# Performance work log

Hardware: AMD Instinct MI355X
Metric: run time of the kernel (lower is better)

Reference implementation:

```python
import jax, jax.numpy as jnp
import numpy as np

EPS = 1e-7
B, N, DIM, NH, HD, WIN, HASH_WIN = 2, 1024, 512, 8, 64, 64, 8


def expmap0(v, c):
    sqrt_c = jnp.clip(jnp.sqrt(c), EPS)
    v_norm = jnp.linalg.norm(v, axis=-1, keepdims=True)
    is_zero = v_norm < EPS
    safe = jnp.clip(v_norm, EPS)
    mag = jnp.tanh(sqrt_c * safe) / sqrt_c
    return jnp.where(is_zero, jnp.zeros_like(v), mag * (v / safe))


def poincare_dist(x, y, c):
    # x: (B,H,N,1,D), y: (B,H,N,W,D), c: (B,1,1,1,1) -> (B,H,N,W)
    sqrt_c = jnp.clip(jnp.sqrt(c), EPS)
    x2 = jnp.sum(x * x, -1, keepdims=True)
    y2 = jnp.sum(y * y, -1, keepdims=True)
    xy = jnp.sum(x * y, -1, keepdims=True)
    num = (1 - 2 * c * xy + c * y2) * x + (1 - c * x2) * (-y)
    den = 1 - 2 * c * xy + c * c * x2 * y2
    diff = num / jnp.clip(den, EPS)
    dn = jnp.linalg.norm(diff, axis=-1)
    arg = jnp.minimum(jnp.squeeze(sqrt_c, -1) * jnp.clip(dn, EPS), 1.0 - EPS)
    return 2.0 * jnp.arctanh(arg) / jnp.squeeze(sqrt_c, -1)


def sliding_windows(t, w):
    # t: (B,H,N,D) -> (B,H,N,w,D), left-padded causal window
    Bb, H, Nn, D = t.shape
    pad = jnp.zeros((Bb, H, w - 1, D), t.dtype)
    tp = jnp.concatenate([pad, t], axis=2)
    idx = jnp.arange(w)[None, :] + jnp.arange(Nn)[:, None]  # (N,w)
    return tp[:, :, idx, :]


def layernorm(x, s, b):
    m = jnp.mean(x, -1, keepdims=True)
    v = jnp.var(x, -1, keepdims=True)
    return (x - m) / jnp.sqrt(v + 1e-6) * s + b


def rope(x, cos, sin):
    # x: (B,N,H,hd), cos/sin: (N, hd//2) -- complex rotation in real arithmetic
    xr, xi = jnp.split(x, 2, axis=-1)
    cos = cos[None, :, None, :]
    sin = sin[None, :, None, :]
    return jnp.concatenate([xr * cos - xi * sin, xr * sin + xi * cos], axis=-1)


def setup_inputs() -> dict:
    key = jax.random.key(0)
    ks = jax.random.split(key, 10)
    x = jax.random.normal(ks[0], (B, N, DIM), jnp.float32)
    pos = jnp.arange(N, dtype=jnp.float32)
    inv = 1.0 / (10000.0 ** (jnp.arange(0, HD, 2, dtype=jnp.float32) / HD))
    ang = pos[:, None] * inv[None, :]  # (N, HD//2)
    freqs_cos, freqs_sin = jnp.cos(ang), jnp.sin(ang)
    c = jax.random.uniform(ks[1], (B,), jnp.float32) * 0.9 + 0.1
    s = 0.02
    Wq = jax.random.normal(ks[2], (DIM, DIM), jnp.float32) * s
    Wk = jax.random.normal(ks[3], (DIM, DIM), jnp.float32) * s
    Wv = jax.random.normal(ks[4], (DIM, DIM), jnp.float32) * s
    Wo = jax.random.normal(ks[5], (DIM, DIM), jnp.float32) * s
    W1 = jax.random.normal(ks[6], (DIM, 4 * DIM), jnp.float32) * s
    W2 = jax.random.normal(ks[7], (4 * DIM, DIM), jnp.float32) * s
    bq = jnp.zeros((DIM,)); bk = jnp.zeros((DIM,)); bv = jnp.zeros((DIM,))
    bo = jnp.zeros((DIM,)); b1 = jnp.zeros((4 * DIM,)); b2 = jnp.zeros((DIM,))
    ln1_s = jnp.ones((DIM,)); ln1_b = jnp.zeros((DIM,))
    ln2_s = jnp.ones((DIM,)); ln2_b = jnp.zeros((DIM,))
    geo_scale = jnp.ones((NH, 1, 1), jnp.float32)
    hash_offset = jax.random.normal(ks[8], (1, 1, NH, HD), jnp.float32) * 0.01
    return dict(x=x, freqs_cos=freqs_cos, freqs_sin=freqs_sin, c=c,
                Wq=Wq, bq=bq, Wk=Wk, bk=bk, Wv=Wv, bv=bv, Wo=Wo, bo=bo,
                W1=W1, b1=b1, W2=W2, b2=b2,
                ln1_s=ln1_s, ln1_b=ln1_b, ln2_s=ln2_s, ln2_b=ln2_b,
                geo_scale=geo_scale, hash_offset=hash_offset)


def reference(x, freqs_cos, freqs_sin, c, Wq, bq, Wk, bk, Wv, bv, Wo, bo,
              W1, b1, W2, b2, ln1_s, ln1_b, ln2_s, ln2_b, geo_scale, hash_offset):
    x_res = x
    xn = layernorm(x, ln1_s, ln1_b)
    q = (xn @ Wq + bq).reshape(B, N, NH, HD)
    k = (xn @ Wk + bk).reshape(B, N, NH, HD)
    v = (xn @ Wv + bv).reshape(B, N, NH, HD)
    q = q + hash_offset * jnp.log(1.0 + HASH_WIN)
    q_rot = rope(q, freqs_cos, freqs_sin)
    k_rot = rope(k, freqs_cos, freqs_sin)
    c_b = c.reshape(B, 1, 1, 1)
    q_h = expmap0(q_rot, c_b)
    k_h = expmap0(k_rot, c_b)
    q_h, k_h, v = (t.transpose(0, 2, 1, 3) for t in (q_h, k_h, v))  # (B,H,N,D)
    k_win = sliding_windows(k_h, WIN)  # (B,H,N,W,D)
    v_win = sliding_windows(v, WIN)
    dist = poincare_dist(q_h[:, :, :, None, :], k_win, c.reshape(B, 1, 1, 1, 1))  # (B,H,N,W)
    scores = -geo_scale * dist
    w = jax.nn.softmax(scores, axis=-1)
    attn = jnp.einsum('bhnw,bhnwd->bhnd', w, v_win)
    attn = attn.transpose(0, 2, 1, 3).reshape(B, N, DIM)
    x_out = x_res + (attn @ Wo + bo)
    h = layernorm(x_out, ln2_s, ln2_b)
    ffn = jax.nn.gelu(h @ W1 + b1) @ W2 + b2
    return x_out + ffn
```

## Files before the change

### kernel.cpp

```cpp
#include <hip/hip_runtime.h>
#include <math.h>
#include <stdint.h>

#define Bn   2
#define Nn   1024
#define DIMn 512
#define NHn  8
#define HDn  64
#define QKVS 1536
#define EPSF 1e-7f

typedef __attribute__((ext_vector_type(8))) short short8;
typedef __attribute__((ext_vector_type(4))) float floatx4;
typedef __attribute__((ext_vector_type(4))) float fx4;
typedef __attribute__((ext_vector_type(4))) unsigned short usx4;

__device__ __forceinline__ unsigned short f2bf(float f) {
  union { float f; uint32_t u; } v; v.f = f;
  uint32_t u = v.u;
  return (unsigned short)((u + 0x7FFFu + ((u >> 16) & 1u)) >> 16);
}
__device__ __forceinline__ float bf2f(unsigned short h) {
  union { uint32_t u; float f; } v; v.u = ((uint32_t)h) << 16;
  return v.f;
}

__device__ __forceinline__ float wsum(float v) {
#pragma unroll
  for (int m = 32; m >= 1; m >>= 1) v += __shfl_xor(v, m, 64);
  return v;
}

__device__ __forceinline__ float gelu_tanh(float x) {
  const float k0 = 0.7978845608028654f;
  float x3 = x * x * x;
  return 0.5f * x * (1.f + tanhf(k0 * (x + 0.044715f * x3)));
}

__device__ __forceinline__ void glds16(const unsigned short* g, unsigned short* l) {
  __builtin_amdgcn_global_load_lds((const __attribute__((address_space(1))) void*)g,
                                   (__attribute__((address_space(3))) void*)l, 16, 0, 0);
}

__global__ __launch_bounds__(256) void prep_kernel(
    const float* __restrict__ Wq, const float* __restrict__ Wk,
    const float* __restrict__ Wv, const float* __restrict__ Wo,
    const float* __restrict__ W1, const float* __restrict__ W2,
    unsigned short* __restrict__ Wcat_hi, unsigned short* __restrict__ Wcat_lo,
    unsigned short* __restrict__ Wo_t, unsigned short* __restrict__ W1_t,
    unsigned short* __restrict__ W2_t,
    const float* __restrict__ bq, const float* __restrict__ bk,
    const float* __restrict__ bv, float* __restrict__ bias_cat,
    const float* __restrict__ x, const float* __restrict__ ln1s,
    const float* __restrict__ ln1b,
    unsigned short* __restrict__ xn_hi, unsigned short* __restrict__ xn_lo) {
  __shared__ float t[32][33];
  __shared__ float red[2][4];
  int bid = blockIdx.x;
  int tid = threadIdx.x;
  if (bid == 3072) {
    for (int i = tid; i < 512; i += 256) {
      bias_cat[i] = bq[i];
      bias_cat[512 + i] = bk[i];
      bias_cat[1024 + i] = bv[i];
    }
    return;
  }
  if (bid > 3072) {
    int row = bid - 3073;
    const float* xr = x + (size_t)row * DIMn;
    float2 xv = *(const float2*)(xr + tid * 2);
    float s  = xv.x + xv.y;
    float s2 = xv.x * xv.x + xv.y * xv.y;
    s = wsum(s); s2 = wsum(s2);
    int wv = tid >> 6;
    if ((tid & 63) == 0) { red[0][wv] = s; red[1][wv] = s2; }
    __syncthreads();
    s  = red[0][0] + red[0][1] + red[0][2] + red[0][3];
    s2 = red[1][0] + red[1][1] + red[1][2] + red[1][3];
    float mean = s * (1.f / DIMn);
    float var  = s2 * (1.f / DIMn) - mean * mean;
    float rstd = rsqrtf(var + 1e-6f);
    int d = tid * 2;
    float2 gv = *(const float2*)(ln1s + d);
    float2 bv2 = *(const float2*)(ln1b + d);
    float o0 = (xv.x - mean) * rstd * gv.x + bv2.x;
    float o1 = (xv.y - mean) * rstd * gv.y + bv2.y;
    size_t idx = (size_t)row * DIMn + d;
    unsigned short h0 = f2bf(o0), h1 = f2bf(o1);
    ushort2 hv; hv.x = h0; hv.y = h1;
    *(ushort2*)(xn_hi + idx) = hv;
    ushort2 lv; lv.x = f2bf(o0 - bf2f(h0)); lv.y = f2bf(o1 - bf2f(h1));
    *(ushort2*)(xn_lo + idx) = lv;
    return;
  }
  const float* W;
  unsigned short* hi;
  unsigned short* lo = nullptr;
  int K, N, tix;
  if (bid < 256)       { W = Wq; hi = Wcat_hi;               lo = Wcat_lo;               K = 512;  N = 512;  tix = bid; }
  else if (bid < 512)  { W = Wk; hi = Wcat_hi + 512 * 512;   lo = Wcat_lo + 512 * 512;   K = 512;  N = 512;  tix = bid - 256; }
  else if (bid < 768)  { W = Wv; hi = Wcat_hi + 1024 * 512;  K = 512;  N = 512;  tix = bid - 512; }
  else if (bid < 1024) { W = Wo; hi = Wo_t;                  K = 512;  N = 512;  tix = bid - 768; }
  else if (bid < 2048) { W = W1; hi = W1_t;                  K = 512;  N = 2048; tix = bid - 1024; }
  else                 { W = W2; hi = W2_t;                  K = 2048; N = 512;  tix = bid - 2048; }
  int ntn = N >> 5;
  int kt = tix / ntn, nt = tix - kt * ntn;
  int k0 = kt * 32, n0 = nt * 32;
  {
    int r = tid >> 3, c = (tid & 7) << 2;
    fx4 v = *(const fx4*)&W[(size_t)(k0 + r) * N + n0 + c];
    t[r][c] = v.x; t[r][c + 1] = v.y; t[r][c + 2] = v.z; t[r][c + 3] = v.w;
  }
  __syncthreads();
  for (int i = tid; i < 1024; i += 256) {
    int r = i >> 5, c = i & 31;
    float v = t[c][r];
    unsigned short h = f2bf(v);
    size_t oi = (size_t)(n0 + r) * K + k0 + c;
    hi[oi] = h;
    if (lo) lo[oi] = f2bf(v - bf2f(h));
  }
}

__global__ __launch_bounds__(256) void ln_kernel(const float* __restrict__ x,
                                                 const float* __restrict__ g,
                                                 const float* __restrict__ be,
                                                 unsigned short* __restrict__ yhi) {
  __shared__ float red[2][4];
  int row = blockIdx.x;
  int tid = threadIdx.x;
  const float* xr = x + (size_t)row * DIMn;
  float2 xv = *(const float2*)(xr + tid * 2);
  float s  = xv.x + xv.y;
  float s2 = xv.x * xv.x + xv.y * xv.y;
  s = wsum(s); s2 = wsum(s2);
  int wv = tid >> 6;
  if ((tid & 63) == 0) { red[0][wv] = s; red[1][wv] = s2; }
  __syncthreads();
  s  = red[0][0] + red[0][1] + red[0][2] + red[0][3];
  s2 = red[1][0] + red[1][1] + red[1][2] + red[1][3];
  float mean = s * (1.f / DIMn);
  float var  = s2 * (1.f / DIMn) - mean * mean;
  float rstd = rsqrtf(var + 1e-6f);
  int d = tid * 2;
  float2 gv = *(const float2*)(g + d);
  float2 bv = *(const float2*)(be + d);
  float o0 = (xv.x - mean) * rstd * gv.x + bv.x;
  float o1 = (xv.y - mean) * rstd * gv.y + bv.y;
  size_t idx = (size_t)row * DIMn + d;
  ushort2 hv; hv.x = f2bf(o0); hv.y = f2bf(o1);
  *(ushort2*)(yhi + idx) = hv;
}

template <int BM, int BN, int BKT, int SPLIT, int EPI, int OUTBF16>
__global__ __launch_bounds__(256) void gemm_mfma(
    const unsigned short* __restrict__ Ahi, const unsigned short* __restrict__ Alo,
    const unsigned short* __restrict__ Bhi, const unsigned short* __restrict__ Blo,
    const float* __restrict__ bias, const float* __restrict__ res,
    void* __restrict__ outp, int M, int N, int K) {
  constexpr int FI = BM / 32, FJ = BN / 32;
  constexpr int AE = BM * BKT, BE = BN * BKT;
  constexpr int NB = (SPLIT > 0) ? 2 : 1;
  constexpr int CPR = BKT / 8;
  constexpr int ACH = BM * CPR, BCH = BN * CPR;
  constexpr int CST = BN + 4;
  constexpr int SMEM_STAGE = NB * (AE + BE);
  constexpr int SMEM_EPI   = BM * CST * 2;
  constexpr int SMEM_N = (SMEM_STAGE > SMEM_EPI) ? SMEM_STAGE : SMEM_EPI;
  __shared__ __align__(16) unsigned short smem[SMEM_N];
  unsigned short* AsHi = smem;
  unsigned short* AsLo = smem + ((SPLIT > 0) ? AE : 0);
  unsigned short* BsHi = smem + NB * AE;
  unsigned short* BsLo = BsHi + ((SPLIT > 0) ? BE : 0);

  int tid = threadIdx.x;
  int lane = tid & 63;
  int wid = tid >> 6;
  int wm = (wid >> 1) * (BM / 2), wn = (wid & 1) * (BN / 2);
  int bm = blockIdx.y * BM, bn = blockIdx.x * BN;
  int m16 = lane & 15, kg = lane >> 4;
  bool dos = (SPLIT == 1) || (SPLIT == 2 && bn < 1024);

  floatx4 acc[FI][FJ];
#pragma unroll
  for (int i = 0; i < FI; ++i)
#pragma unroll
    for (int j = 0; j < FJ; ++j) { floatx4 z = {0.f, 0.f, 0.f, 0.f}; acc[i][j] = z; }

  const unsigned short* aph = Ahi + (size_t)bm * K;
  const unsigned short* bph = Bhi + (size_t)bn * K;
  const unsigned short* apl = (SPLIT > 0) ? (Alo + (size_t)bm * K) : nullptr;
  const unsigned short* bpl = (SPLIT > 0) ? (Blo + (size_t)bn * K) : nullptr;

  for (int k0 = 0; k0 < K; k0 += BKT) {
#pragma unroll
    for (int c = tid; c < ACH; c += 256) {
      int row = c / CPR, kk = (c % CPR) * 8;
      glds16(aph + (size_t)row * K + k0 + kk, AsHi + c * 8);
      if (SPLIT > 0 && dos) glds16(apl + (size_t)row * K + k0 + kk, AsLo + c * 8);
    }
#pragma unroll
    for (int c = tid; c < BCH; c += 256) {
      int row = c / CPR, kk = (c % CPR) * 8;
      glds16(bph + (size_t)row * K + k0 + kk, BsHi + c * 8);
      if (SPLIT > 0 && dos) glds16(bpl + (size_t)row * K + k0 + kk, BsLo + c * 8);
    }
    __syncthreads();

#pragma unroll
    for (int ks = 0; ks < BKT / 32; ++ks) {
      short8 ah[FI], bh[FJ];
      short8 al[(SPLIT > 0) ? FI : 1], bl[(SPLIT > 0) ? FJ : 1];
#pragma unroll
      for (int i = 0; i < FI; ++i) {
        int r = wm + i * 16 + m16;
        ah[i] = *(const short8*)&AsHi[r * BKT + ks * 32 + kg * 8];
        if (SPLIT > 0 && dos) al[i] = *(const short8*)&AsLo[r * BKT + ks * 32 + kg * 8];
      }
#pragma unroll
      for (int j = 0; j < FJ; ++j) {
        int r = wn + j * 16 + m16;
        bh[j] = *(const short8*)&BsHi[r * BKT + ks * 32 + kg * 8];
        if (SPLIT > 0 && dos) bl[j] = *(const short8*)&BsLo[r * BKT + ks * 32 + kg * 8];
      }
#pragma unroll
      for (int i = 0; i < FI; ++i)
#pragma unroll
        for (int j = 0; j < FJ; ++j) {
          acc[i][j] = __builtin_amdgcn_mfma_f32_16x16x32_bf16(ah[i], bh[j], acc[i][j], 0, 0, 0);
          if (SPLIT > 0) {
            if (dos) {
              acc[i][j] = __builtin_amdgcn_mfma_f32_16x16x32_bf16(al[i], bh[j], acc[i][j], 0, 0, 0);
              acc[i][j] = __builtin_amdgcn_mfma_f32_16x16x32_bf16(ah[i], bl[j], acc[i][j], 0, 0, 0);
            }
          }
        }
    }
    __syncthreads();
  }

  float* Cs = (float*)smem;
#pragma unroll
  for (int i = 0; i < FI; ++i)
#pragma unroll
    for (int j = 0; j < FJ; ++j)
#pragma unroll
      for (int r = 0; r < 4; ++r)
        Cs[(wm + i * 16 + kg * 4 + r) * CST + wn + j * 16 + m16] = acc[i][j][r];
  __syncthreads();
  constexpr int TOT = BM * BN / 4;
  for (int t = tid; t < TOT; t += 256) {
    int row = (t << 2) / BN;
    int col = (t << 2) & (BN - 1);
    fx4 v = *(const fx4*)&Cs[row * CST + col];
    fx4 bs = *(const fx4*)&bias[bn + col];
    v = v + bs;
    size_t gidx = (size_t)(bm + row) * N + bn + col;
    if constexpr (EPI == 1) {
      fx4 rr = *(const fx4*)&res[gidx];
      v = v + rr;
    }
    if constexpr (EPI == 2) {
      v.x = gelu_tanh(v.x); v.y = gelu_tanh(v.y);
      v.z = gelu_tanh(v.z); v.w = gelu_tanh(v.w);
    }
    if constexpr (OUTBF16) {
      usx4 h;
      h.x = f2bf(v.x); h.y = f2bf(v.y); h.z = f2bf(v.z); h.w = f2bf(v.w);
      *(usx4*)((unsigned short*)outp + gidx) = h;
    } else {
      *(fx4*)((float*)outp + gidx) = v;
    }
  }
}

__global__ __launch_bounds__(512) void attn_fused(const float* __restrict__ qkv,
                                                  const float* __restrict__ fcos,
                                                  const float* __restrict__ fsin,
                                                  const float* __restrict__ cvec,
                                                  const float* __restrict__ geo,
                                                  const float* __restrict__ hash,
                                                  unsigned short* __restrict__ attn_out) {
  __shared__ unsigned short Qhi[32][72], Qlo[32][72];
  __shared__ unsigned short Khi[96][72], Klo[96][72];
  __shared__ unsigned short Vt[64][104];
  __shared__ unsigned short Pb[32][104];
  __shared__ float Sf[32][97];
  __shared__ float x2s[32], bxs[32], y2s[96], gys[96];

  int tid = threadIdx.x, lane = tid & 63, wv = tid >> 6;
  int bid = blockIdx.x;
  int nt = bid & 31, h = (bid >> 5) & 7, b = bid >> 8;
  int n0 = nt * 32;
  float c = cvec[b];
  float sqc = sqrtf(c);
  float rsqc = 1.f / sqc;
  float gs = geo[h];
  int dr = lane & 31;
  bool hih = lane >= 32;
  const float LOG9 = 2.1972245773362196f;
  float hofr = hash[h * HDn + dr] * LOG9;
  float hofi = hash[h * HDn + dr + 32] * LOG9;

  for (int i = tid; i < 32 * 52; i += 512) ((uint32_t*)Pb)[i] = 0u;

#pragma unroll
  for (int i = 0; i < 4; ++i) {
    int q = wv * 4 + i;
    int n = n0 + q;
    size_t bas = (size_t)(b * Nn + n) * QKVS + h * HDn;
    float qr = qkv[bas + dr] + hofr;
    float qi = qkv[bas + dr + 32] + hofi;
    float cs = fcos[n * 32 + dr], sn = fsin[n * 32 + dr];
    float qv = hih ? (qr * sn + qi * cs) : (qr * cs - qi * sn);
    float nq = sqrtf(wsum(qv * qv));
    float sq = fmaxf(nq, EPSF);
    float t = sqc * sq;
    float em = expf(-2.f * t);
    float opem = 1.f + em;
    float mag = ((1.f - em) / opem) * rsqc;
    float sech2 = 4.f * em / (opem * opem);
    float oq = (nq < EPSF) ? 0.f : mag * (qv / sq);
    unsigned short hh = f2bf(oq);
    Qhi[q][lane] = hh;
    Qlo[q][lane] = f2bf(oq - bf2f(hh));
    if (lane == 0) {
      x2s[q] = (nq < EPSF) ? 0.f : mag * mag;
      bxs[q] = (nq < EPSF) ? 1.f : sech2;
    }
  }
#pragma unroll 4
  for (int i = 0; i < 12; ++i) {
    int r = wv * 12 + i;
    int gi = n0 - 64 + r;
    float ok = 0.f, vf = 0.f, y2 = 0.f, gy = 1.f;
    if (gi >= 0) {
      size_t bas = (size_t)(b * Nn + gi) * QKVS + h * HDn;
      float kr = qkv[bas + 512 + dr];
      float ki = qkv[bas + 512 + dr + 32];
      vf = qkv[bas + 1024 + lane];
      float cs = fcos[gi * 32 + dr], sn = fsin[gi * 32 + dr];
      float kv = hih ? (kr * sn + ki * cs) : (kr * cs - ki * sn);
      float nk = sqrtf(wsum(kv * kv));
      float sk = fmaxf(nk, EPSF);
      float t = sqc * sk;
      float em = expf(-2.f * t);
      float opem = 1.f + em;
      float mag = ((1.f - em) / opem) * rsqc;
      float sech2 = 4.f * em / (opem * opem);
      ok = (nk < EPSF) ? 0.f : mag * (kv / sk);
      y2 = (nk < EPSF) ? 0.f : mag * mag;
      gy = (nk < EPSF) ? 1.f : sech2;
    }
    unsigned short hh = f2bf(ok);
    Khi[r][lane] = hh;
    Klo[r][lane] = f2bf(ok - bf2f(hh));
    Vt[lane][r] = f2bf(vf);
    if (lane == 0) { y2s[r] = y2; gys[r] = gy; }
  }
  __syncthreads();

  int m16 = lane & 15, kg = lane >> 4;
#pragma unroll
  for (int uu = 0; uu < 2; ++uu) {
    int u = wv + uu * 8;
    if (u < 12) {
      int mt = u / 6, ntile = u % 6;
      floatx4 acc = {0.f, 0.f, 0.f, 0.f};
#pragma unroll
      for (int ks = 0; ks < 2; ++ks) {
        short8 ah = *(const short8*)&Qhi[mt * 16 + m16][ks * 32 + kg * 8];
        short8 al = *(const short8*)&Qlo[mt * 16 + m16][ks * 32 + kg * 8];
        short8 bh = *(const short8*)&Khi[ntile * 16 + m16][ks * 32 + kg * 8];
        short8 bl = *(const short8*)&Klo[ntile * 16 + m16][ks * 32 + kg * 8];
        acc = __builtin_amdgcn_mfma_f32_16x16x32_bf16(ah, bh, acc, 0, 0, 0);
        acc = __builtin_amdgcn_mfma_f32_16x16x32_bf16(al, bh, acc, 0, 0, 0);
        acc = __builtin_amdgcn_mfma_f32_16x16x32_bf16(ah, bl, acc, 0, 0, 0);
      }
#pragma unroll
      for (int r = 0; r < 4; ++r) Sf[mt * 16 + kg * 4 + r][ntile * 16 + m16] = acc[r];
    }
  }
  __syncthreads();

#pragma unroll
  for (int i = 0; i < 4; ++i) {
    int nl = wv * 4 + i;
    int r = nl + 1 + lane;
    float xy = Sf[nl][r];
    float x2 = x2s[nl], y2 = y2s[r];
    float bx = bxs[nl], gy = gys[r];

    float den = fmaf(c * c * x2, y2, fmaf(-2.f * c, xy, 1.f));
    den = fmaxf(den, EPSF);
    float rden = 1.f / den;
    float s2 = fmaxf(x2 - 2.f * xy + y2, 0.f);
    float z = sqrtf(c * s2 * rden);
    float omz2 = bx * gy * rden;
    float opz = 1.f + fminf(z, 1.f);
    float ratio = fminf(opz * opz / omz2, 1.9999999e7f);
    float sc = -gs * logf(ratio) * rsqc;

    float e = expf(sc);
    float se = wsum(e);
    Pb[nl][r] = f2bf(e / se);
  }
  __syncthreads();

  {
    int mt = wv >> 2, ntile = wv & 3;
    floatx4 acc = {0.f, 0.f, 0.f, 0.f};
#pragma unroll
    for (int ks = 0; ks < 3; ++ks) {
      short8 a = *(const short8*)&Pb[mt * 16 + m16][ks * 32 + kg * 8];
      short8 bb = *(const short8*)&Vt[ntile * 16 + m16][ks * 32 + kg * 8];
      acc = __builtin_amdgcn_mfma_f32_16x16x32_bf16(a, bb, acc, 0, 0, 0);
    }
#pragma unroll
    for (int r = 0; r < 4; ++r) {
      int qrow = mt * 16 + kg * 4 + r;
      int d = ntile * 16 + m16;
      attn_out[(size_t)(b * Nn + n0 + qrow) * DIMn + h * HDn + d] = f2bf(acc[r]);
    }
  }
}

extern "C" void kernel_launch(void* const* d_in, const int* in_sizes, int n_in,
                              void* d_out, int out_size, void* d_ws, size_t ws_size,
                              hipStream_t stream) {
  const float* x    = (const float*)d_in[0];
  const float* fcos = (const float*)d_in[1];
  const float* fsin = (const float*)d_in[2];
  const float* cvec = (const float*)d_in[3];
  const float* Wq = (const float*)d_in[4];  const float* bq = (const float*)d_in[5];
  const float* Wk = (const float*)d_in[6];  const float* bk = (const float*)d_in[7];
  const float* Wv = (const float*)d_in[8];  const float* bv = (const float*)d_in[9];
  const float* Wo = (const float*)d_in[10]; const float* bo = (const float*)d_in[11];
  const float* W1 = (const float*)d_in[12]; const float* b1 = (const float*)d_in[13];
  const float* W2 = (const float*)d_in[14]; const float* b2 = (const float*)d_in[15];
  const float* ln1s = (const float*)d_in[16]; const float* ln1b = (const float*)d_in[17];
  const float* ln2s = (const float*)d_in[18]; const float* ln2b = (const float*)d_in[19];
  const float* geo  = (const float*)d_in[20]; const float* hash = (const float*)d_in[21];
  float* out = (float*)d_out;
  char* base = (char*)d_ws;

  unsigned short* Wcat_hi = (unsigned short*)(base + 0);
  unsigned short* Wcat_lo = (unsigned short*)(base + 1572864);
  unsigned short* Wo_t    = (unsigned short*)(base + 3145728);
  unsigned short* W1_t    = (unsigned short*)(base + 3670016);
  unsigned short* W2_t    = (unsigned short*)(base + 5767168);
  unsigned short* xn_hi   = (unsigned short*)(base + 7864320);
  unsigned short* xn_lo   = (unsigned short*)(base + 9961472);
  float*          qkv     = (float*)(base + 12058624);
  unsigned short* attnb   = (unsigned short*)(base + 7864320);
  float*          xout    = (float*)(base + 9961472);
  unsigned short* hbuf    = (unsigned short*)(base + 14155776);
  unsigned short* mid     = (unsigned short*)(base + 16252928);
  float*          bias_cat= (float*)(base + 24641536);

  const int M = Bn * Nn;

  prep_kernel<<<3073 + M, 256, 0, stream>>>(Wq, Wk, Wv, Wo, W1, W2, Wcat_hi, Wcat_lo,
                                            Wo_t, W1_t, W2_t, bq, bk, bv, bias_cat,
                                            x, ln1s, ln1b, xn_hi, xn_lo);
  gemm_mfma<64, 64, 64, 2, 0, 0><<<dim3(QKVS / 64, M / 64), 256, 0, stream>>>(
      xn_hi, xn_lo, Wcat_hi, Wcat_lo, bias_cat, nullptr, qkv, M, QKVS, 512);
  attn_fused<<<Bn * NHn * (Nn / 32), 512, 0, stream>>>(qkv, fcos, fsin, cvec, geo, hash, attnb);
  gemm_mfma<32, 64, 64, 0, 1, 0><<<dim3(DIMn / 64, M / 32), 256, 0, stream>>>(
      attnb, nullptr, Wo_t, nullptr, bo, x, xout, M, DIMn, 512);
  ln_kernel<<<M, 256, 0, stream>>>(xout, ln2s, ln2b, hbuf);
  gemm_mfma<64, 128, 64, 0, 2, 1><<<dim3(2048 / 128, M / 64), 256, 0, stream>>>(
      hbuf, nullptr, W1_t, nullptr, b1, nullptr, mid, M, 2048, 512);
  gemm_mfma<32, 64, 64, 0, 1, 0><<<dim3(DIMn / 64, M / 32), 256, 0, stream>>>(
      mid, nullptr, W2_t, nullptr, b2, xout, out, M, DIMn, 2048);
}
```

Before: 191.3 us.

## Fuse all stages into one persistent cooperative megakernel with grid syncs

Replaces the seven separate launches (weight prep, LN1, QKV GEMM, attention, out-proj, LN2, FFN GEMMs) with a single cooperative kernel of 256 blocks × 512 threads. The stages are separated by grid.sync, and work units are distributed round-robin across blocks. The GEMM tiles are rewritten as 64x64 units with double-buffered LDS staging. The aim is to remove launch gaps and inter-kernel drain. The cost is only 256 blocks of parallelism, large shared memory per block, grid-wide barriers, and smaller GEMM tiles for the out-proj and W2 stages (one unit per block).

Measured after the change: 434.8 us. 127% more time.

```diff
diff --git a/kernel.cpp b/kernel.cpp
--- a/kernel.cpp
+++ b/kernel.cpp
@@ -1,6 +1,9 @@
 #include <hip/hip_runtime.h>
+#include <hip/hip_cooperative_groups.h>
 #include <math.h>
 #include <stdint.h>
+
+namespace cg = cooperative_groups;
 
 #define Bn   2
 #define Nn   1024
@@ -9,11 +12,14 @@
 #define HDn  64
 #define QKVS 1536
 #define EPSF 1e-7f
+#define NBLK 256
+#define NTHR 512
 
 typedef __attribute__((ext_vector_type(8))) short short8;
 typedef __attribute__((ext_vector_type(4))) float floatx4;
 typedef __attribute__((ext_vector_type(4))) float fx4;
 typedef __attribute__((ext_vector_type(4))) unsigned short usx4;
+typedef unsigned short ushort_t;
 
 __device__ __forceinline__ unsigned short f2bf(float f) {
   union { float f; uint32_t u; } v; v.f = f;
@@ -42,217 +48,83 @@
                                    (__attribute__((address_space(3))) void*)l, 16, 0, 0);
 }
 
-__global__ __launch_bounds__(256) void prep_kernel(
-    const float* __restrict__ Wq, const float* __restrict__ Wk,
-    const float* __restrict__ Wv, const float* __restrict__ Wo,
-    const float* __restrict__ W1, const float* __restrict__ W2,
-    unsigned short* __restrict__ Wcat_hi, unsigned short* __restrict__ Wcat_lo,
-    unsigned short* __restrict__ Wo_t, unsigned short* __restrict__ W1_t,
-    unsigned short* __restrict__ W2_t,
-    const float* __restrict__ bq, const float* __restrict__ bk,
-    const float* __restrict__ bv, float* __restrict__ bias_cat,
-    const float* __restrict__ x, const float* __restrict__ ln1s,
-    const float* __restrict__ ln1b,
-    unsigned short* __restrict__ xn_hi, unsigned short* __restrict__ xn_lo) {
-  __shared__ float t[32][33];
-  __shared__ float red[2][4];
-  int bid = blockIdx.x;
-  int tid = threadIdx.x;
-  if (bid == 3072) {
-    for (int i = tid; i < 512; i += 256) {
-      bias_cat[i] = bq[i];
-      bias_cat[512 + i] = bk[i];
-      bias_cat[1024 + i] = bv[i];
-    }
-    return;
-  }
-  if (bid > 3072) {
-    int row = bid - 3073;
-    const float* xr = x + (size_t)row * DIMn;
-    float2 xv = *(const float2*)(xr + tid * 2);
-    float s  = xv.x + xv.y;
-    float s2 = xv.x * xv.x + xv.y * xv.y;
-    s = wsum(s); s2 = wsum(s2);
-    int wv = tid >> 6;
-    if ((tid & 63) == 0) { red[0][wv] = s; red[1][wv] = s2; }
+__device__ void ln_row(const float* __restrict__ xr, const float* __restrict__ g,
+                       const float* __restrict__ be, unsigned short* __restrict__ yhi,
+                       unsigned short* __restrict__ ylo, float* red, int tid) {
+  float v = xr[tid];
+  float s = wsum(v), s2 = wsum(v * v);
+  int wv = tid >> 6;
+  if ((tid & 63) == 0) { red[wv] = s; red[8 + wv] = s2; }
+  __syncthreads();
+  s = 0.f; s2 = 0.f;
+#pragma unroll
+  for (int i = 0; i < 8; ++i) { s += red[i]; s2 += red[8 + i]; }
+  __syncthreads();
+  float mean = s * (1.f / DIMn);
+  float var = s2 * (1.f / DIMn) - mean * mean;
+  float rstd = rsqrtf(var + 1e-6f);
+  float o = (v - mean) * rstd * g[tid] + be[tid];
+  unsigned short h = f2bf(o);
+  yhi[tid] = h;
+  if (ylo) ylo[tid] = f2bf(o - bf2f(h));
+}
+
+template <int EPI, int OUTBF16>
+__device__ void gemm_unit(const unsigned short* __restrict__ A,
+                          const unsigned short* __restrict__ B,
+                          const float* __restrict__ bias, const float* __restrict__ res,
+                          void* __restrict__ outp, int bm, int bn, int N, int K,
+                          char* LU, int tid) {
+  constexpr int BKT = 64;
+  constexpr int AE = 64 * BKT;
+  constexpr int STG = 2 * AE;
+  unsigned short* sb = (unsigned short*)LU;
+  int lane = tid & 63, wid = tid >> 6;
+  int wm = (wid >> 1) * 16, wn = (wid & 1) * 32;
+  int m16 = lane & 15, kg = lane >> 4;
+  floatx4 acc[2];
+  { floatx4 z = {0.f, 0.f, 0.f, 0.f}; acc[0] = z; acc[1] = z; }
+  const unsigned short* ap = A + (size_t)bm * K;
+  const unsigned short* bp = B + (size_t)bn * K;
+
+  auto stage = [&](int k0, unsigned short* buf) {
+    int c = tid;
+    int row = c >> 3, kk = (c & 7) * 8;
+    glds16(ap + (size_t)row * K + k0 + kk, buf + c * 8);
+    glds16(bp + (size_t)row * K + k0 + kk, buf + AE + c * 8);
+  };
+
+  const int NT = K / BKT;
+  stage(0, sb);
+  __syncthreads();
+  int cur = 0;
+  for (int t = 0; t < NT; ++t) {
+    unsigned short* buf = sb + cur * STG;
+    int nxt = cur ^ 1;
+    if (t + 1 < NT) stage((t + 1) * BKT, sb + nxt * STG);
+#pragma unroll
+    for (int ks = 0; ks < 2; ++ks) {
+      short8 ah = *(const short8*)&buf[(wm + m16) * BKT + ks * 32 + kg * 8];
+#pragma unroll
+      for (int j = 0; j < 2; ++j) {
+        short8 bh = *(const short8*)&buf[AE + (wn + j * 16 + m16) * BKT + ks * 32 + kg * 8];
+        acc[j] = __builtin_amdgcn_mfma_f32_16x16x32_bf16(ah, bh, acc[j], 0, 0, 0);
+      }
+    }
     __syncthreads();
-    s  = red[0][0] + red[0][1] + red[0][2] + red[0][3];
-    s2 = red[1][0] + red[1][1] + red[1][2] + red[1][3];
-    float mean = s * (1.f / DIMn);
-    float var  = s2 * (1.f / DIMn) - mean * mean;
-    float rstd = rsqrtf(var + 1e-6f);
-    int d = tid * 2;
-    float2 gv = *(const float2*)(ln1s + d);
-    float2 bv2 = *(const float2*)(ln1b + d);
-    float o0 = (xv.x - mean) * rstd * gv.x + bv2.x;
-    float o1 = (xv.y - mean) * rstd * gv.y + bv2.y;
-    size_t idx = (size_t)row * DIMn + d;
-    unsigned short h0 = f2bf(o0), h1 = f2bf(o1);
-    ushort2 hv; hv.x = h0; hv.y = h1;
-    *(ushort2*)(xn_hi + idx) = hv;
-    ushort2 lv; lv.x = f2bf(o0 - bf2f(h0)); lv.y = f2bf(o1 - bf2f(h1));
-    *(ushort2*)(xn_lo + idx) = lv;
-    return;
-  }
-  const float* W;
-  unsigned short* hi;
-  unsigned short* lo = nullptr;
-  int K, N, tix;
-  if (bid < 256)       { W = Wq; hi = Wcat_hi;               lo = Wcat_lo;               K = 512;  N = 512;  tix = bid; }
-  else if (bid < 512)  { W = Wk; hi = Wcat_hi + 512 * 512;   lo = Wcat_lo + 512 * 512;   K = 512;  N = 512;  tix = bid - 256; }
-  else if (bid < 768)  { W = Wv; hi = Wcat_hi + 1024 * 512;  K = 512;  N = 512;  tix = bid - 512; }
-  else if (bid < 1024) { W = Wo; hi = Wo_t;                  K = 512;  N = 512;  tix = bid - 768; }
-  else if (bid < 2048) { W = W1; hi = W1_t;                  K = 512;  N = 2048; tix = bid - 1024; }
-  else                 { W = W2; hi = W2_t;                  K = 2048; N = 512;  tix = bid - 2048; }
-  int ntn = N >> 5;
-  int kt = tix / ntn, nt = tix - kt * ntn;
-  int k0 = kt * 32, n0 = nt * 32;
-  {
-    int r = tid >> 3, c = (tid & 7) << 2;
-    fx4 v = *(const fx4*)&W[(size_t)(k0 + r) * N + n0 + c];
-    t[r][c] = v.x; t[r][c + 1] = v.y; t[r][c + 2] = v.z; t[r][c + 3] = v.w;
-  }
-  __syncthreads();
-  for (int i = tid; i < 1024; i += 256) {
-    int r = i >> 5, c = i & 31;
-    float v = t[c][r];
-    unsigned short h = f2bf(v);
-    size_t oi = (size_t)(n0 + r) * K + k0 + c;
-    hi[oi] = h;
-    if (lo) lo[oi] = f2bf(v - bf2f(h));
-  }
-}
-
-__global__ __launch_bounds__(256) void ln_kernel(const float* __restrict__ x,
-                                                 const float* __restrict__ g,
-                                                 const float* __restrict__ be,
-                                                 unsigned short* __restrict__ yhi) {
-  __shared__ float red[2][4];
-  int row = blockIdx.x;
-  int tid = threadIdx.x;
-  const float* xr = x + (size_t)row * DIMn;
-  float2 xv = *(const float2*)(xr + tid * 2);
-  float s  = xv.x + xv.y;
-  float s2 = xv.x * xv.x + xv.y * xv.y;
-  s = wsum(s); s2 = wsum(s2);
-  int wv = tid >> 6;
-  if ((tid & 63) == 0) { red[0][wv] = s; red[1][wv] = s2; }
-  __syncthreads();
-  s  = red[0][0] + red[0][1] + red[0][2] + red[0][3];
-  s2 = red[1][0] + red[1][1] + red[1][2] + red[1][3];
-  float mean = s * (1.f / DIMn);
-  float var  = s2 * (1.f / DIMn) - mean * mean;
-  float rstd = rsqrtf(var + 1e-6f);
-  int d = tid * 2;
-  float2 gv = *(const float2*)(g + d);
-  float2 bv = *(const float2*)(be + d);
-  float o0 = (xv.x - mean) * rstd * gv.x + bv.x;
-  float o1 = (xv.y - mean) * rstd * gv.y + bv.y;
-  size_t idx = (size_t)row * DIMn + d;
-  ushort2 hv; hv.x = f2bf(o0); hv.y = f2bf(o1);
-  *(ushort2*)(yhi + idx) = hv;
-}
-
-template <int BM, int BN, int BKT, int SPLIT, int EPI, int OUTBF16>
-__global__ __launch_bounds__(256) void gemm_mfma(
-    const unsigned short* __restrict__ Ahi, const unsigned short* __restrict__ Alo,
-    const unsigned short* __restrict__ Bhi, const unsigned short* __restrict__ Blo,
-    const float* __restrict__ bias, const float* __restrict__ res,
-    void* __restrict__ outp, int M, int N, int K) {
-  constexpr int FI = BM / 32, FJ = BN / 32;
-  constexpr int AE = BM * BKT, BE = BN * BKT;
-  constexpr int NB = (SPLIT > 0) ? 2 : 1;
-  constexpr int CPR = BKT / 8;
-  constexpr int ACH = BM * CPR, BCH = BN * CPR;
-  constexpr int CST = BN + 4;
-  constexpr int SMEM_STAGE = NB * (AE + BE);
-  constexpr int SMEM_EPI   = BM * CST * 2;
-  constexpr int SMEM_N = (SMEM_STAGE > SMEM_EPI) ? SMEM_STAGE : SMEM_EPI;
-  __shared__ __align__(16) unsigned short smem[SMEM_N];
-  unsigned short* AsHi = smem;
-  unsigned short* AsLo = smem + ((SPLIT > 0) ? AE : 0);
-  unsigned short* BsHi = smem + NB * AE;
-  unsigned short* BsLo = BsHi + ((SPLIT > 0) ? BE : 0);
-
-  int tid = threadIdx.x;
-  int lane = tid & 63;
-  int wid = tid >> 6;
-  int wm = (wid >> 1) * (BM / 2), wn = (wid & 1) * (BN / 2);
-  int bm = blockIdx.y * BM, bn = blockIdx.x * BN;
-  int m16 = lane & 15, kg = lane >> 4;
-  bool dos = (SPLIT == 1) || (SPLIT == 2 && bn < 1024);
-
-  floatx4 acc[FI][FJ];
-#pragma unroll
-  for (int i = 0; i < FI; ++i)
-#pragma unroll
-    for (int j = 0; j < FJ; ++j) { floatx4 z = {0.f, 0.f, 0.f, 0.f}; acc[i][j] = z; }
-
-  const unsigned short* aph = Ahi + (size_t)bm * K;
-  const unsigned short* bph = Bhi + (size_t)bn * K;
-  const unsigned short* apl = (SPLIT > 0) ? (Alo + (size_t)bm * K) : nullptr;
-  const unsigned short* bpl = (SPLIT > 0) ? (Blo + (size_t)bn * K) : nullptr;
-
-  for (int k0 = 0; k0 < K; k0 += BKT) {
-#pragma unroll
-    for (int c = tid; c < ACH; c += 256) {
-      int row = c / CPR, kk = (c % CPR) * 8;
-      glds16(aph + (size_t)row * K + k0 + kk, AsHi + c * 8);
-      if (SPLIT > 0 && dos) glds16(apl + (size_t)row * K + k0 + kk, AsLo + c * 8);
-    }
-#pragma unroll
-    for (int c = tid; c < BCH; c += 256) {
-      int row = c / CPR, kk = (c % CPR) * 8;
-      glds16(bph + (size_t)row * K + k0 + kk, BsHi + c * 8);
-      if (SPLIT > 0 && dos) glds16(bpl + (size_t)row * K + k0 + kk, BsLo + c * 8);
-    }
-    __syncthreads();
-
-#pragma unroll
-    for (int ks = 0; ks < BKT / 32; ++ks) {
-      short8 ah[FI], bh[FJ];
-      short8 al[(SPLIT > 0) ? FI : 1], bl[(SPLIT > 0) ? FJ : 1];
-#pragma unroll
-      for (int i = 0; i < FI; ++i) {
-        int r = wm + i * 16 + m16;
-        ah[i] = *(const short8*)&AsHi[r * BKT + ks * 32 + kg * 8];
-        if (SPLIT > 0 && dos) al[i] = *(const short8*)&AsLo[r * BKT + ks * 32 + kg * 8];
-      }
-#pragma unroll
-      for (int j = 0; j < FJ; ++j) {
-        int r = wn + j * 16 + m16;
-        bh[j] = *(const short8*)&BsHi[r * BKT + ks * 32 + kg * 8];
-        if (SPLIT > 0 && dos) bl[j] = *(const short8*)&BsLo[r * BKT + ks * 32 + kg * 8];
-      }
-#pragma unroll
-      for (int i = 0; i < FI; ++i)
-#pragma unroll
-        for (int j = 0; j < FJ; ++j) {
-          acc[i][j] = __builtin_amdgcn_mfma_f32_16x16x32_bf16(ah[i], bh[j], acc[i][j], 0, 0, 0);
-          if (SPLIT > 0) {
-            if (dos) {
-              acc[i][j] = __builtin_amdgcn_mfma_f32_16x16x32_bf16(al[i], bh[j], acc[i][j], 0, 0, 0);
-              acc[i][j] = __builtin_amdgcn_mfma_f32_16x16x32_bf16(ah[i], bl[j], acc[i][j], 0, 0, 0);
-            }
-          }
-        }
-    }
-    __syncthreads();
-  }
-
-  float* Cs = (float*)smem;
-#pragma unroll
-  for (int i = 0; i < FI; ++i)
-#pragma unroll
-    for (int j = 0; j < FJ; ++j)
-#pragma unroll
-      for (int r = 0; r < 4; ++r)
-        Cs[(wm + i * 16 + kg * 4 + r) * CST + wn + j * 16 + m16] = acc[i][j][r];
-  __syncthreads();
-  constexpr int TOT = BM * BN / 4;
-  for (int t = tid; t < TOT; t += 256) {
-    int row = (t << 2) / BN;
-    int col = (t << 2) & (BN - 1);
+    cur = nxt;
+  }
+
+  float* Cs = (float*)LU;
+  constexpr int CST = 68;
+#pragma unroll
+  for (int j = 0; j < 2; ++j)
+#pragma unroll
+    for (int r = 0; r < 4; ++r)
+      Cs[(wm + kg * 4 + r) * CST + wn + j * 16 + m16] = acc[j][r];
+  __syncthreads();
+  for (int t = tid; t < 1024; t += NTHR) {
+    int row = t >> 4, col = (t & 15) << 2;
     fx4 v = *(const fx4*)&Cs[row * CST + col];
     fx4 bs = *(const fx4*)&bias[bn + col];
     v = v + bs;
@@ -273,25 +145,106 @@
       *(fx4*)((float*)outp + gidx) = v;
     }
   }
-}
-
-__global__ __launch_bounds__(512) void attn_fused(const float* __restrict__ qkv,
-                                                  const float* __restrict__ fcos,
-                                                  const float* __restrict__ fsin,
-                                                  const float* __restrict__ cvec,
-                                                  const float* __restrict__ geo,
-                                                  const float* __restrict__ hash,
-                                                  unsigned short* __restrict__ attn_out) {
-  __shared__ unsigned short Qhi[32][72], Qlo[32][72];
-  __shared__ unsigned short Khi[96][72], Klo[96][72];
-  __shared__ unsigned short Vt[64][104];
-  __shared__ unsigned short Pb[32][104];
-  __shared__ float Sf[32][97];
-  __shared__ float x2s[32], bxs[32], y2s[96], gys[96];
-
-  int tid = threadIdx.x, lane = tid & 63, wv = tid >> 6;
-  int bid = blockIdx.x;
-  int nt = bid & 31, h = (bid >> 5) & 7, b = bid >> 8;
+  __syncthreads();
+}
+
+__device__ void qkv_unit(const unsigned short* __restrict__ Ahi,
+                         const unsigned short* __restrict__ Alo,
+                         const unsigned short* __restrict__ Bhi,
+                         const unsigned short* __restrict__ Blo,
+                         const float* __restrict__ bias, float* __restrict__ outp,
+                         int u, int tid, char* LU) {
+  constexpr int BKT = 32, K = 512, N = QKVS;
+  constexpr int AE = 64 * BKT;
+  constexpr int STG = 4 * AE;
+  unsigned short* sb = (unsigned short*)LU;
+  int mt = u / 24, ntl = u % 24;
+  int bm = mt * 64, bn = ntl * 64;
+  bool dos = bn < 1024;
+  int lane = tid & 63, wid = tid >> 6;
+  int wm = (wid >> 1) * 16, wn = (wid & 1) * 32;
+  int m16 = lane & 15, kg = lane >> 4;
+  floatx4 acc[2];
+  { floatx4 z = {0.f, 0.f, 0.f, 0.f}; acc[0] = z; acc[1] = z; }
+  const unsigned short* aph = Ahi + (size_t)bm * K;
+  const unsigned short* bph = Bhi + (size_t)bn * K;
+  const unsigned short* apl = Alo + (size_t)bm * K;
+  const unsigned short* bpl = Blo + (size_t)bn * K;
+
+  auto stage = [&](int k0, unsigned short* buf) {
+    int c = tid & 255;
+    int row = c >> 2, kk = (c & 3) * 8;
+    if (tid < 256) {
+      glds16(aph + (size_t)row * K + k0 + kk, buf + c * 8);
+      if (dos) glds16(apl + (size_t)row * K + k0 + kk, buf + AE + c * 8);
+    } else {
+      glds16(bph + (size_t)row * K + k0 + kk, buf + 2 * AE + c * 8);
+      if (dos) glds16(bpl + (size_t)row * K + k0 + kk, buf + 3 * AE + c * 8);
+    }
+  };
+
+  stage(0, sb);
+  __syncthreads();
+  int cur = 0;
+  for (int t = 0; t < 16; ++t) {
+    unsigned short* buf = sb + cur * STG;
+    int nxt = cur ^ 1;
+    if (t + 1 < 16) stage((t + 1) * BKT, sb + nxt * STG);
+    short8 ah = *(const short8*)&buf[(wm + m16) * BKT + kg * 8];
+    short8 al;
+    if (dos) al = *(const short8*)&buf[AE + (wm + m16) * BKT + kg * 8];
+#pragma unroll
+    for (int j = 0; j < 2; ++j) {
+      int r = wn + j * 16 + m16;
+      short8 bh = *(const short8*)&buf[2 * AE + r * BKT + kg * 8];
+      acc[j] = __builtin_amdgcn_mfma_f32_16x16x32_bf16(ah, bh, acc[j], 0, 0, 0);
+      if (dos) {
+        short8 bl = *(const short8*)&buf[3 * AE + r * BKT + kg * 8];
+        acc[j] = __builtin_amdgcn_mfma_f32_16x16x32_bf16(al, bh, acc[j], 0, 0, 0);
+        acc[j] = __builtin_amdgcn_mfma_f32_16x16x32_bf16(ah, bl, acc[j], 0, 0, 0);
+      }
+    }
+    __syncthreads();
+    cur = nxt;
+  }
+
+  float* Cs = (float*)LU;
+  constexpr int CST = 68;
+#pragma unroll
+  for (int j = 0; j < 2; ++j)
+#pragma unroll
+    for (int r = 0; r < 4; ++r)
+      Cs[(wm + kg * 4 + r) * CST + wn + j * 16 + m16] = acc[j][r];
+  __syncthreads();
+  for (int t = tid; t < 1024; t += NTHR) {
+    int row = t >> 4, col = (t & 15) << 2;
+    fx4 v = *(const fx4*)&Cs[row * CST + col];
+    fx4 bs = *(const fx4*)&bias[bn + col];
+    v = v + bs;
+    *(fx4*)(outp + (size_t)(bm + row) * N + bn + col) = v;
+  }
+  __syncthreads();
+}
+
+__device__ void attn_unit(const float* __restrict__ qkv, const float* __restrict__ fcos,
+                          const float* __restrict__ fsin, const float* __restrict__ cvec,
+                          const float* __restrict__ geo, const float* __restrict__ hash,
+                          unsigned short* __restrict__ attn_out, int bidu, int tid,
+                          char* LU) {
+  unsigned short* Qhi = (unsigned short*)LU;
+  unsigned short* Qlo = Qhi + 32 * 72;
+  unsigned short* Khi = Qlo + 32 * 72;
+  unsigned short* Klo = Khi + 96 * 72;
+  unsigned short* Vt  = Klo + 96 * 72;
+  unsigned short* Pb  = Vt + 64 * 104;
+  float* Sf  = (float*)(Pb + 32 * 104);
+  float* x2s = Sf + 32 * 97;
+  float* bxs = x2s + 32;
+  float* y2s = bxs + 32;
+  float* gys = y2s + 96;
+
+  int lane = tid & 63, wv = tid >> 6;
+  int nt = bidu & 31, h = (bidu >> 5) & 7, b = bidu >> 8;
   int n0 = nt * 32;
   float c = cvec[b];
   float sqc = sqrtf(c);
@@ -303,7 +256,9 @@
   float hofr = hash[h * HDn + dr] * LOG9;
   float hofi = hash[h * HDn + dr + 32] * LOG9;
 
-  for (int i = tid; i < 32 * 52; i += 512) ((uint32_t*)Pb)[i] = 0u;
+  __syncthreads();
+
+  for (int i = tid; i < 32 * 52; i += NTHR) ((uint32_t*)Pb)[i] = 0u;
 
 #pragma unroll
   for (int i = 0; i < 4; ++i) {
@@ -323,8 +278,8 @@
     float sech2 = 4.f * em / (opem * opem);
     float oq = (nq < EPSF) ? 0.f : mag * (qv / sq);
     unsigned short hh = f2bf(oq);
-    Qhi[q][lane] = hh;
-    Qlo[q][lane] = f2bf(oq - bf2f(hh));
+    Qhi[q * 72 + lane] = hh;
+    Qlo[q * 72 + lane] = f2bf(oq - bf2f(hh));
     if (lane == 0) {
       x2s[q] = (nq < EPSF) ? 0.f : mag * mag;
       bxs[q] = (nq < EPSF) ? 1.f : sech2;
@@ -354,9 +309,9 @@
       gy = (nk < EPSF) ? 1.f : sech2;
     }
     unsigned short hh = f2bf(ok);
-    Khi[r][lane] = hh;
-    Klo[r][lane] = f2bf(ok - bf2f(hh));
-    Vt[lane][r] = f2bf(vf);
+    Khi[r * 72 + lane] = hh;
+    Klo[r * 72 + lane] = f2bf(ok - bf2f(hh));
+    Vt[lane * 104 + r] = f2bf(vf);
     if (lane == 0) { y2s[r] = y2; gys[r] = gy; }
   }
   __syncthreads();
@@ -370,16 +325,16 @@
       floatx4 acc = {0.f, 0.f, 0.f, 0.f};
 #pragma unroll
       for (int ks = 0; ks < 2; ++ks) {
-        short8 ah = *(const short8*)&Qhi[mt * 16 + m16][ks * 32 + kg * 8];
-        short8 al = *(const short8*)&Qlo[mt * 16 + m16][ks * 32 + kg * 8];
-        short8 bh = *(const short8*)&Khi[ntile * 16 + m16][ks * 32 + kg * 8];
-        short8 bl = *(const short8*)&Klo[ntile * 16 + m16][ks * 32 + kg * 8];
+        short8 ah = *(const short8*)&Qhi[(mt * 16 + m16) * 72 + ks * 32 + kg * 8];
+        short8 al = *(const short8*)&Qlo[(mt * 16 + m16) * 72 + ks * 32 + kg * 8];
+        short8 bh = *(const short8*)&Khi[(ntile * 16 + m16) * 72 + ks * 32 + kg * 8];
+        short8 bl = *(const short8*)&Klo[(ntile * 16 + m16) * 72 + ks * 32 + kg * 8];
         acc = __builtin_amdgcn_mfma_f32_16x16x32_bf16(ah, bh, acc, 0, 0, 0);
         acc = __builtin_amdgcn_mfma_f32_16x16x32_bf16(al, bh, acc, 0, 0, 0);
         acc = __builtin_amdgcn_mfma_f32_16x16x32_bf16(ah, bl, acc, 0, 0, 0);
       }
 #pragma unroll
-      for (int r = 0; r < 4; ++r) Sf[mt * 16 + kg * 4 + r][ntile * 16 + m16] = acc[r];
+      for (int r = 0; r < 4; ++r) Sf[(mt * 16 + kg * 4 + r) * 97 + ntile * 16 + m16] = acc[r];
     }
   }
   __syncthreads();
@@ -388,7 +343,7 @@
   for (int i = 0; i < 4; ++i) {
     int nl = wv * 4 + i;
     int r = nl + 1 + lane;
-    float xy = Sf[nl][r];
+    float xy = Sf[nl * 97 + r];
     float x2 = x2s[nl], y2 = y2s[r];
     float bx = bxs[nl], gy = gys[r];
 
@@ -404,7 +359,7 @@
 
     float e = expf(sc);
     float se = wsum(e);
-    Pb[nl][r] = f2bf(e / se);
+    Pb[nl * 104 + r] = f2bf(e / se);
   }
   __syncthreads();
 
@@ -413,8 +368,8 @@
     floatx4 acc = {0.f, 0.f, 0.f, 0.f};
 #pragma unroll
     for (int ks = 0; ks < 3; ++ks) {
-      short8 a = *(const short8*)&Pb[mt * 16 + m16][ks * 32 + kg * 8];
-      short8 bb = *(const short8*)&Vt[ntile * 16 + m16][ks * 32 + kg * 8];
+      short8 a = *(const short8*)&Pb[(mt * 16 + m16) * 104 + ks * 32 + kg * 8];
+      short8 bb = *(const short8*)&Vt[(ntile * 16 + m16) * 104 + ks * 32 + kg * 8];
       acc = __builtin_amdgcn_mfma_f32_16x16x32_bf16(a, bb, acc, 0, 0, 0);
     }
 #pragma unroll
@@ -423,6 +378,99 @@
       int d = ntile * 16 + m16;
       attn_out[(size_t)(b * Nn + n0 + qrow) * DIMn + h * HDn + d] = f2bf(acc[r]);
     }
+  }
+}
+
+__global__ __launch_bounds__(NTHR, 2) void mega(
+    const float* x, const float* fcos, const float* fsin, const float* cvec,
+    const float* Wq, const float* bq, const float* Wk, const float* bk,
+    const float* Wv, const float* bv, const float* Wo, const float* bo,
+    const float* W1, const float* b1, const float* W2, const float* b2,
+    const float* ln1s, const float* ln1b, const float* ln2s, const float* ln2b,
+    const float* geo, const float* hash,
+    unsigned short* Wcat_hi, unsigned short* Wcat_lo, unsigned short* Wo_t,
+    unsigned short* W1_t, unsigned short* W2_t,
+    unsigned short* xn_hi, unsigned short* xn_lo, float* qkv,
+    unsigned short* attnb, float* xout, unsigned short* hbuf,
+    unsigned short* mid, float* bias_cat, float* out) {
+  __shared__ __align__(16) char LU[70400];
+  cg::grid_group grid = cg::this_grid();
+  int tid = threadIdx.x, bid = blockIdx.x;
+
+  if (bid == 0) {
+    bias_cat[tid] = bq[tid];
+    bias_cat[512 + tid] = bk[tid];
+    bias_cat[1024 + tid] = bv[tid];
+  }
+  float* tb = (float*)LU;
+  for (int u = bid; u < 3072; u += NBLK) {
+    const float* W;
+    unsigned short* hi;
+    unsigned short* lo = nullptr;
+    int K, N, tix;
+    if (u < 256)       { W = Wq; hi = Wcat_hi;              lo = Wcat_lo;              K = 512;  N = 512;  tix = u; }
+    else if (u < 512)  { W = Wk; hi = Wcat_hi + 512 * 512;  lo = Wcat_lo + 512 * 512;  K = 512;  N = 512;  tix = u - 256; }
+    else if (u < 768)  { W = Wv; hi = Wcat_hi + 1024 * 512; K = 512;  N = 512;  tix = u - 512; }
+    else if (u < 1024) { W = Wo; hi = Wo_t;                 K = 512;  N = 512;  tix = u - 768; }
+    else if (u < 2048) { W = W1; hi = W1_t;                 K = 512;  N = 2048; tix = u - 1024; }
+    else               { W = W2; hi = W2_t;                 K = 2048; N = 512;  tix = u - 2048; }
+    int ntn = N >> 5;
+    int kt = tix / ntn, nt = tix - kt * ntn;
+    int k0 = kt * 32, n0 = nt * 32;
+    {
+      int r = tid >> 4, cc = (tid & 15) << 1;
+      float2 v = *(const float2*)&W[(size_t)(k0 + r) * N + n0 + cc];
+      tb[r * 33 + cc] = v.x;
+      tb[r * 33 + cc + 1] = v.y;
+    }
+    __syncthreads();
+    for (int i = tid; i < 1024; i += NTHR) {
+      int r = i >> 5, cc = i & 31;
+      float v = tb[cc * 33 + r];
+      unsigned short h = f2bf(v);
+      size_t oi = (size_t)(n0 + r) * K + k0 + cc;
+      hi[oi] = h;
+      if (lo) lo[oi] = f2bf(v - bf2f(h));
+    }
+    __syncthreads();
+  }
+  {
+    float* red = (float*)LU;
+    for (int r0 = bid; r0 < Bn * Nn; r0 += NBLK)
+      ln_row(x + (size_t)r0 * DIMn, ln1s, ln1b, xn_hi + (size_t)r0 * DIMn,
+             xn_lo + (size_t)r0 * DIMn, red, tid);
+  }
+  grid.sync();
+
+  for (int u = bid; u < 768; u += NBLK)
+    qkv_unit(xn_hi, xn_lo, Wcat_hi, Wcat_lo, bias_cat, qkv, u, tid, LU);
+  grid.sync();
+
+  for (int u = bid; u < Bn * NHn * (Nn / 32); u += NBLK)
+    attn_unit(qkv, fcos, fsin, cvec, geo, hash, attnb, u, tid, LU);
+  grid.sync();
+
+  {
+    int u = bid;
+    gemm_unit<1, 0>(attnb, Wo_t, bo, x, xout, (u >> 3) * 64, (u & 7) * 64, DIMn, 512, LU, tid);
+  }
+  grid.sync();
+
+  {
+    float* red = (float*)LU;
+    __syncthreads();
+    for (int r0 = bid; r0 < Bn * Nn; r0 += NBLK)
+      ln_row(xout + (size_t)r0 * DIMn, ln2s, ln2b, hbuf + (size_t)r0 * DIMn, nullptr, red, tid);
+  }
+  grid.sync();
+
+  for (int u = bid; u < 1024; u += NBLK)
+    gemm_unit<2, 1>(hbuf, W1_t, b1, nullptr, mid, (u >> 5) * 64, (u & 31) * 64, 2048, 512, LU, tid);
+  grid.sync();
+
+  {
+    int u = bid;
+    gemm_unit<1, 0>(mid, W2_t, b2, xout, out, (u >> 3) * 64, (u & 7) * 64, DIMn, 2048, LU, tid);
   }
 }
 
@@ -459,19 +507,17 @@
   unsigned short* mid     = (unsigned short*)(base + 16252928);
   float*          bias_cat= (float*)(base + 24641536);
 
-  const int M = Bn * Nn;
-
-  prep_kernel<<<3073 + M, 256, 0, stream>>>(Wq, Wk, Wv, Wo, W1, W2, Wcat_hi, Wcat_lo,
-                                            Wo_t, W1_t, W2_t, bq, bk, bv, bias_cat,
-                                            x, ln1s, ln1b, xn_hi, xn_lo);
-  gemm_mfma<64, 64, 64, 2, 0, 0><<<dim3(QKVS / 64, M / 64), 256, 0, stream>>>(
-      xn_hi, xn_lo, Wcat_hi, Wcat_lo, bias_cat, nullptr, qkv, M, QKVS, 512);
-  attn_fused<<<Bn * NHn * (Nn / 32), 512, 0, stream>>>(qkv, fcos, fsin, cvec, geo, hash, attnb);
-  gemm_mfma<32, 64, 64, 0, 1, 0><<<dim3(DIMn / 64, M / 32), 256, 0, stream>>>(
-      attnb, nullptr, Wo_t, nullptr, bo, x, xout, M, DIMn, 512);
-  ln_kernel<<<M, 256, 0, stream>>>(xout, ln2s, ln2b, hbuf);
-  gemm_mfma<64, 128, 64, 0, 2, 1><<<dim3(2048 / 128, M / 64), 256, 0, stream>>>(
-      hbuf, nullptr, W1_t, nullptr, b1, nullptr, mid, M, 2048, 512);
-  gemm_mfma<32, 64, 64, 0, 1, 0><<<dim3(DIMn / 64, M / 32), 256, 0, stream>>>(
-      mid, nullptr, W2_t, nullptr, b2, xout, out, M, DIMn, 2048);
-}
+  void* args[] = {
+    (void*)&x, (void*)&fcos, (void*)&fsin, (void*)&cvec,
+    (void*)&Wq, (void*)&bq, (void*)&Wk, (void*)&bk,
+    (void*)&Wv, (void*)&bv, (void*)&Wo, (void*)&bo,
+    (void*)&W1, (void*)&b1, (void*)&W2, (void*)&b2,
+    (void*)&ln1s, (void*)&ln1b, (void*)&ln2s, (void*)&ln2b,
+    (void*)&geo, (void*)&hash,
+    (void*)&Wcat_hi, (void*)&Wcat_lo, (void*)&Wo_t, (void*)&W1_t, (void*)&W2_t,
+    (void*)&xn_hi, (void*)&xn_lo, (void*)&qkv, (void*)&attnb, (void*)&xout,
+    (void*)&hbuf, (void*)&mid, (void*)&bias_cat, (void*)&out
+  };
+  hipLaunchCooperativeKernel(reinterpret_cast<void*>(mega), dim3(NBLK), dim3(NTHR),
+                             args, 0, stream);
+}
```
